# Kernel tuning notes

Hardware: AMD Instinct MI355X
Metric: run time of the kernel (lower is better)

## Reference

```python
import jax, jax.numpy as jnp
import numpy as np
from jax.ops import segment_sum, segment_max

N, E, H, C = 20000, 320000, 4, 128
G, NF, EF, GF = 1024, 9, 4, 50
EPS = 1e-5
NEG_SLOPE = 0.2


def setup_inputs() -> dict:
    key = jax.random.key(0)
    ks = jax.random.split(key, 16)
    inp = {
        'x': jax.random.normal(ks[0], (N, NF), jnp.float32),
        'edge_attr': jax.random.normal(ks[1], (E, EF), jnp.float32),
        'global_feat': jax.random.normal(ks[2], (G, GF), jnp.float32),
        'Wl1': jax.random.normal(ks[3], (NF, H * C), jnp.float32) * 0.1,
        'Wr1': jax.random.normal(ks[4], (NF, H * C), jnp.float32) * 0.1,
        'We1': jax.random.normal(ks[5], (EF, H * C), jnp.float32) * 0.1,
        'att1': jax.random.normal(ks[6], (H, C), jnp.float32) * 0.1,
        'b1': jax.random.normal(ks[7], (H * C,), jnp.float32) * 0.01,
        'gamma1': jnp.ones((H * C,), jnp.float32),
        'beta1': jnp.zeros((H * C,), jnp.float32),
        'mean1': jnp.zeros((H * C,), jnp.float32),
        'var1': jnp.ones((H * C,), jnp.float32),
        'Wl2': jax.random.normal(ks[8], (H * C, H * C), jnp.float32) * 0.05,
        'Wr2': jax.random.normal(ks[9], (H * C, H * C), jnp.float32) * 0.05,
        'We2': jax.random.normal(ks[10], (EF, H * C), jnp.float32) * 0.1,
        'att2': jax.random.normal(ks[11], (H, C), jnp.float32) * 0.1,
        'b2': jax.random.normal(ks[12], (H * C,), jnp.float32) * 0.01,
        'gamma2': jnp.ones((H * C,), jnp.float32),
        'beta2': jnp.zeros((H * C,), jnp.float32),
        'mean2': jnp.zeros((H * C,), jnp.float32),
        'var2': jnp.ones((H * C,), jnp.float32),
        'fc1_w': jax.random.normal(ks[13], (H * C + GF, C), jnp.float32) * 0.05,
        'fc1_b': jnp.zeros((C,), jnp.float32),
        'fc2_w': jax.random.normal(ks[14], (C, 1), jnp.float32) * 0.1,
        'fc2_b': jnp.zeros((1,), jnp.float32),
        'edge_index': jax.random.randint(ks[15], (2, E), 0, N, jnp.int32),
        'batch': jnp.sort(jax.random.randint(jax.random.fold_in(key, 99), (N,), 0, G, jnp.int32)),
    }
    return inp


def gatv2_layer(x, src, dst, ea, Wl, Wr, We, att, bias):
    # PyG GATv2Conv: add self-loops with fill_value='mean' edge_attr
    n = x.shape[0]
    loop = jnp.arange(n, dtype=src.dtype)
    deg = segment_sum(jnp.ones((src.shape[0],), x.dtype), dst, num_segments=n)
    ea_mean = segment_sum(ea, dst, num_segments=n) / jnp.clip(deg, 1.0)[:, None]
    s = jnp.concatenate([src, loop])
    d = jnp.concatenate([dst, loop])
    eat = jnp.concatenate([ea, ea_mean], axis=0)
    xl = (x @ Wl).reshape(n, H, C)  # source transform
    xr = (x @ Wr).reshape(n, H, C)  # target transform
    ee = (eat @ We).reshape(-1, H, C)
    e = jax.nn.leaky_relu(xl[s] + xr[d] + ee, NEG_SLOPE)  # [E+N, H, C]
    logits = jnp.einsum('ehc,hc->eh', e, att)  # [E+N, H]
    m = segment_max(logits, d, num_segments=n)  # stable segment softmax
    ex = jnp.exp(logits - m[d])
    alpha = ex / segment_sum(ex, d, num_segments=n)[d]
    out = segment_sum(alpha[..., None] * xl[s], d, num_segments=n)  # [N, H, C]
    return out.reshape(n, H * C) + bias


def batch_norm(x, g, b, mu, var):
    return (x - mu) * jax.lax.rsqrt(var + EPS) * g + b


def reference(x, edge_attr, global_feat, Wl1, Wr1, We1, att1, b1, gamma1, beta1, mean1, var1,
              Wl2, Wr2, We2, att2, b2, gamma2, beta2, mean2, var2,
              fc1_w, fc1_b, fc2_w, fc2_b, edge_index, batch):
    src, dst = edge_index[0], edge_index[1]
    h = jax.nn.relu(batch_norm(gatv2_layer(x, src, dst, edge_attr, Wl1, Wr1, We1, att1, b1),
                               gamma1, beta1, mean1, var1))
    h = jax.nn.relu(batch_norm(gatv2_layer(h, src, dst, edge_attr, Wl2, Wr2, We2, att2, b2),
                               gamma2, beta2, mean2, var2))
    cnt = segment_sum(jnp.ones((h.shape[0],), h.dtype), batch, num_segments=G)
    pooled = segment_sum(h, batch, num_segments=G) / jnp.clip(cnt, 1.0)[:, None]  # [G, H*C]
    z = jnp.concatenate([pooled, global_feat], axis=1)
    z = jax.nn.relu(z @ fc1_w + fc1_b)
    return (z @ fc2_w + fc2_b).squeeze()
```

## Files before the change

### kernel.cpp

```cpp
#include <hip/hip_runtime.h>
#include <hip/hip_bf16.h>

#define Nn 20000
#define Ee 320000
#define Hh 4
#define Cc 128
#define HC 512
#define Gg 1024
#define NFt 9
#define EFt 4
#define GFt 50
#define EPSf 1e-5f
#define SLOPE 0.2f

typedef __attribute__((ext_vector_type(8))) short bf16x8;
typedef __attribute__((ext_vector_type(4))) float f32x4;
typedef __attribute__((ext_vector_type(2))) float f32x2;
typedef __attribute__((ext_vector_type(4))) unsigned ui32x4;

typedef const __attribute__((address_space(1))) unsigned char* gp1_t;
typedef __attribute__((address_space(3))) unsigned char* lp3_t;
__device__ __forceinline__ void gload16(const void* g, void* l) {
    __builtin_amdgcn_global_load_lds((gp1_t)g, (lp3_t)l, 16, 0, 0);
}

__device__ __forceinline__ float bf2f(short s) {
    return __uint_as_float(((unsigned)(unsigned short)s) << 16);
}
__device__ __forceinline__ float rfl(float v) {
    return __uint_as_float(__builtin_amdgcn_readfirstlane(__float_as_uint(v)));
}

__device__ __forceinline__ f32x2 pkfma(f32x2 a, f32x2 b, f32x2 c) {
    f32x2 d;
    asm("v_pk_fma_f32 %0, %1, %2, %3" : "=v"(d) : "v"(a), "v"(b), "v"(c));
    return d;
}
__device__ __forceinline__ f32x2 pkadd(f32x2 a, f32x2 b) {
    f32x2 d;
    asm("v_pk_add_f32 %0, %1, %2" : "=v"(d) : "v"(a), "v"(b));
    return d;
}
__device__ __forceinline__ f32x2 pkmul(f32x2 a, f32x2 b) {
    f32x2 d;
    asm("v_pk_mul_f32 %0, %1, %2" : "=v"(d) : "v"(a), "v"(b));
    return d;
}

__global__ void k_setup2(const int* __restrict__ dst, int* __restrict__ deg,
                         const int* __restrict__ batch, int* __restrict__ gofs) {
    int b = blockIdx.x, t = threadIdx.x;
    if (b < 1250) {
        int e = b * 256 + t;
        if (e < Ee) atomicAdd(&deg[dst[e]], 1);
    } else {
        int i = (b - 1250) * 256 + t;
        if (i >= Nn) return;
        int bb = batch[i];
        if (i == 0) {
            for (int g = 0; g <= bb; ++g) gofs[g] = 0;
        } else {
            int bp = batch[i - 1];
            for (int g = bp + 1; g <= bb; ++g) gofs[g] = i;
        }
        if (i == Nn - 1) {
            for (int g = bb + 1; g <= Gg; ++g) gofs[g] = Nn;
        }
    }
}

__global__ __launch_bounds__(256) void k_cvtW(const float* __restrict__ Wl2,
                                              const float* __restrict__ Wr2,
                                              __hip_bfloat16* __restrict__ Wt) {
    __shared__ float tile[64][65];
    int tc = blockIdx.x * 64;
    int tk = blockIdx.y * 64;
    int t = threadIdx.x;
    int lc = t & 63, lr = t >> 6;
    const float* W = (tc < 512) ? Wl2 : Wr2;
    int cb = tc & 511;
#pragma unroll
    for (int i = 0; i < 16; ++i) {
        int r = lr * 16 + i;
        tile[r][lc] = W[(size_t)(tk + r) * 512 + cb + lc];
    }
    __syncthreads();
#pragma unroll
    for (int i = 0; i < 16; ++i) {
        int c = lr * 16 + i;
        Wt[(size_t)(tc + c) * 512 + tk + lc] = __float2bfloat16(tile[lc][c]);
    }
}

__global__ __launch_bounds__(256) void k_xlxr1(const float* __restrict__ x,
                                               const float* __restrict__ Wl1,
                                               const float* __restrict__ Wr1,
                                               __hip_bfloat16* __restrict__ xl,
                                               __hip_bfloat16* __restrict__ xr) {
    int t = threadIdx.x;
    int l = t & 63, w = t >> 6;
    int ch0 = l * 8;
    int wid = blockIdx.x * 4 + w;
    int n0 = wid * 2, n1 = n0 + 1;
    float xa[NFt], xb[NFt];
#pragma unroll
    for (int f = 0; f < NFt; ++f) {
        xa[f] = x[n0 * NFt + f];
        xb[f] = x[n1 * NFt + f];
    }
    float a0[8] = {}, r0[8] = {}, a1[8] = {}, r1[8] = {};
#pragma unroll
    for (int f = 0; f < NFt; ++f) {
        f32x4 wl0 = *(const f32x4*)&Wl1[f * HC + ch0];
        f32x4 wl1 = *(const f32x4*)&Wl1[f * HC + ch0 + 4];
        f32x4 wr0 = *(const f32x4*)&Wr1[f * HC + ch0];
        f32x4 wr1 = *(const f32x4*)&Wr1[f * HC + ch0 + 4];
#pragma unroll
        for (int k = 0; k < 4; ++k) {
            a0[k] = fmaf(xa[f], wl0[k], a0[k]);
            a0[k + 4] = fmaf(xa[f], wl1[k], a0[k + 4]);
            r0[k] = fmaf(xa[f], wr0[k], r0[k]);
            r0[k + 4] = fmaf(xa[f], wr1[k], r0[k + 4]);
            a1[k] = fmaf(xb[f], wl0[k], a1[k]);
            a1[k + 4] = fmaf(xb[f], wl1[k], a1[k + 4]);
            r1[k] = fmaf(xb[f], wr0[k], r1[k]);
            r1[k + 4] = fmaf(xb[f], wr1[k], r1[k + 4]);
        }
    }
    auto cvt8 = [](const float* v) {
        bf16x8 o;
#pragma unroll
        for (int k = 0; k < 8; ++k) {
            union { float f; unsigned u; } cv;
            cv.f = v[k];
            unsigned r = (cv.u + 0x7fff + ((cv.u >> 16) & 1)) >> 16;
            o[k] = (short)r;
        }
        return o;
    };
    *(bf16x8*)(xl + (size_t)n0 * HC + ch0) = cvt8(a0);
    *(bf16x8*)(xr + (size_t)n0 * HC + ch0) = cvt8(r0);
    *(bf16x8*)(xl + (size_t)n1 * HC + ch0) = cvt8(a1);
    *(bf16x8*)(xr + (size_t)n1 * HC + ch0) = cvt8(r1);
}

__global__ void k_scan(const int* __restrict__ deg, int* __restrict__ rowptr) {
    __shared__ int sums[1024];
    int t = threadIdx.x;
    const int n = Nn;
    int chunk = (n + 1023) / 1024;
    int start = t * chunk;
    int lim = min(start + chunk, n);
    int s = 0;
    for (int i = start; i < lim; ++i) s += deg[i];
    sums[t] = s;
    __syncthreads();
    for (int off = 1; off < 1024; off <<= 1) {
        int v = (t >= off) ? sums[t - off] : 0;
        __syncthreads();
        sums[t] += v;
        __syncthreads();
    }
    int run = (t == 0) ? 0 : sums[t - 1];
    for (int i = start; i < lim; ++i) { rowptr[i] = run; run += deg[i]; }
    if (t == 1023) rowptr[n] = sums[1023];
}

__global__ void k_scatter(const int* __restrict__ src, const int* __restrict__ dst,
                          const float* __restrict__ ea, const int* __restrict__ rowptr,
                          int* __restrict__ fill, int* __restrict__ csr_src,
                          float4* __restrict__ ea_s) {
    int e = blockIdx.x * 256 + threadIdx.x;
    if (e >= Ee) return;
    int d = dst[e];
    int pos = rowptr[d] + atomicAdd(&fill[d], 1);
    csr_src[pos] = src[e];
    ea_s[pos] = ((const float4*)ea)[e];
}

__global__ __launch_bounds__(256) void k_gemm_mfma(const short* __restrict__ Abf,
                                                   const short* __restrict__ Bt,
                                                   __hip_bfloat16* __restrict__ xl,
                                                   __hip_bfloat16* __restrict__ xr, int M) {
    __shared__ short As[128 * 32];
    __shared__ short Bs[128 * 32];
    int tid = threadIdx.x;
    int l = tid & 63;
    int wid = tid >> 6;
    int bm0 = blockIdx.x * 128;
    int bn0 = blockIdx.y * 128;
    int wr = (wid >> 1) * 64;
    int wc = (wid & 1) * 64;
    f32x4 acc[4][4] = {};

    int srow = l >> 2;
    int skoff = ((l & 3) ^ ((l >> 3) & 3)) * 8;
    int rk = (((l >> 4) ^ (l >> 1)) & 3) * 8;

    for (int k0 = 0; k0 < 512; k0 += 32) {
        {
            int c = wid;
            long row = min(bm0 + c * 16 + srow, M - 1);
            gload16(Abf + row * 512 + k0 + skoff, &As[c * 512]);
            int col = bn0 + c * 16 + srow;
            gload16(Bt + (size_t)col * 512 + k0 + skoff, &Bs[c * 512]);
            c = wid + 4;
            row = min(bm0 + c * 16 + srow, M - 1);
            gload16(Abf + row * 512 + k0 + skoff, &As[c * 512]);
            col = bn0 + c * 16 + srow;
            gload16(Bt + (size_t)col * 512 + k0 + skoff, &Bs[c * 512]);
        }
        asm volatile("s_waitcnt vmcnt(0)" ::: "memory");
        __syncthreads();
        bf16x8 af[4], bfr[4];
#pragma unroll
        for (int m = 0; m < 4; ++m)
            af[m] = *(const bf16x8*)&As[(wr + m * 16 + (l & 15)) * 32 + rk];
#pragma unroll
        for (int n = 0; n < 4; ++n)
            bfr[n] = *(const bf16x8*)&Bs[(wc + n * 16 + (l & 15)) * 32 + rk];
#pragma unroll
        for (int m = 0; m < 4; ++m)
#pragma unroll
            for (int n = 0; n < 4; ++n)
                acc[m][n] = __builtin_amdgcn_mfma_f32_16x16x32_bf16(af[m], bfr[n],
                                                                    acc[m][n], 0, 0, 0);
        __syncthreads();
    }
    __hip_bfloat16* dst = (bn0 < 512) ? xl : xr;
    int cb = bn0 & 511;
#pragma unroll
    for (int m = 0; m < 4; ++m) {
#pragma unroll
        for (int n = 0; n < 4; ++n) {
            int col = cb + wc + n * 16 + (l & 15);
#pragma unroll
            for (int r = 0; r < 4; ++r) {
                int row = bm0 + wr + m * 16 + (l >> 4) * 4 + r;
                if (row < M) dst[(size_t)row * 512 + col] = __float2bfloat16(acc[m][n][r]);
            }
        }
    }
}

__global__ __launch_bounds__(256) void k_fused_attn(
    const __hip_bfloat16* __restrict__ xl, const __hip_bfloat16* __restrict__ xr,
    const float* __restrict__ We, const float* __restrict__ att,
    const int* __restrict__ rowptr, const int* __restrict__ csr_src,
    const float4* __restrict__ ea_s, const float* __restrict__ bias,
    const float* __restrict__ gamma, const float* __restrict__ beta,
    const float* __restrict__ mean, const float* __restrict__ var,
    __hip_bfloat16* __restrict__ hout) {
    int n = blockIdx.x * 4 + (threadIdx.x >> 6);
    if (n >= Nn) return;
    int l = threadIdx.x & 63;
    int ch0 = l * 8;

    f32x2 wee2[4][4], ar2[4], rr2[4];
#pragma unroll
    for (int f = 0; f < 4; ++f) {
        f32x4 w0 = *(const f32x4*)&We[f * HC + ch0];
        f32x4 w1 = *(const f32x4*)&We[f * HC + ch0 + 4];
        wee2[f][0] = (f32x2){w0.x, w0.y};
        wee2[f][1] = (f32x2){w0.z, w0.w};
        wee2[f][2] = (f32x2){w1.x, w1.y};
        wee2[f][3] = (f32x2){w1.z, w1.w};
    }
    {
        f32x4 a0 = *(const f32x4*)&att[ch0];
        f32x4 a1 = *(const f32x4*)&att[ch0 + 4];
        ar2[0] = (f32x2){a0.x, a0.y};
        ar2[1] = (f32x2){a0.z, a0.w};
        ar2[2] = (f32x2){a1.x, a1.y};
        ar2[3] = (f32x2){a1.z, a1.w};
    }
    {
        ui32x4 ru = *(const ui32x4*)(xr + (size_t)n * HC + ch0);
#pragma unroll
        for (int j = 0; j < 4; ++j) {
            unsigned u = ru[j];
            rr2[j] = (f32x2){__uint_as_float(u << 16), __uint_as_float(u & 0xffff0000u)};
        }
    }

    int start = rowptr[n];
    int nedge = rowptr[n + 1] - start;
    int last = start + nedge - 1;

    float m = -1e30f, den = 0.f;
    f32x2 acc2[4] = {};
    float es0 = 0.f, es1 = 0.f, es2 = 0.f, es3 = 0.f;

    struct Chunk {
        int s[4];
        float e[4][4];
        bf16x8 x[4];
    };

    auto accum4 = [&](const Chunk& c, const float* ex) {
#pragma unroll
        for (int i = 0; i < 4; ++i) {
            f32x2 esp = (f32x2){ex[i], ex[i]};
            ui32x4 xu = *(const ui32x4*)&c.x[i];
#pragma unroll
            for (int j = 0; j < 4; ++j) {
                unsigned u = xu[j];
                f32x2 xv = (f32x2){__uint_as_float(u << 16),
                                   __uint_as_float(u & 0xffff0000u)};
                acc2[j] = pkfma(esp, xv, acc2[j]);
            }
        }
    };

    auto step = [&](Chunk& cur, Chunk& nxt, int base) {
#pragma unroll
        for (int i = 0; i < 4; ++i) {
            int idx = min(start + base + 4 + i, last);
            nxt.s[i] = __builtin_amdgcn_readfirstlane(csr_src[idx]);
            float4 v = ea_s[idx];
            nxt.e[i][0] = rfl(v.x); nxt.e[i][1] = rfl(v.y);
            nxt.e[i][2] = rfl(v.z); nxt.e[i][3] = rfl(v.w);
        }
#pragma unroll
        for (int i = 0; i < 4; ++i)
            nxt.x[i] = *(const bf16x8*)(xl + (size_t)nxt.s[i] * HC + ch0);

#pragma unroll
        for (int i = 0; i < 4; ++i) {
            if (base + i < nedge) {
                es0 += cur.e[i][0]; es1 += cur.e[i][1];
                es2 += cur.e[i][2]; es3 += cur.e[i][3];
            }
        }

        float p[4];
#pragma unroll
        for (int i = 0; i < 4; ++i) {
            ui32x4 xu = *(const ui32x4*)&cur.x[i];
            f32x2 es0p = (f32x2){cur.e[i][0], cur.e[i][0]};
            f32x2 es1p = (f32x2){cur.e[i][1], cur.e[i][1]};
            f32x2 es2p = (f32x2){cur.e[i][2], cur.e[i][2]};
            f32x2 es3p = (f32x2){cur.e[i][3], cur.e[i][3]};
            f32x2 plin = (f32x2){0.f, 0.f}, pabs = (f32x2){0.f, 0.f};
#pragma unroll
            for (int j = 0; j < 4; ++j) {
                unsigned u = xu[j];
                f32x2 xv = (f32x2){__uint_as_float(u << 16),
                                   __uint_as_float(u & 0xffff0000u)};
                f32x2 z = pkadd(xv, rr2[j]);
                z = pkfma(es0p, wee2[0][j], z);
                z = pkfma(es1p, wee2[1][j], z);
                z = pkfma(es2p, wee2[2][j], z);
                z = pkfma(es3p, wee2[3][j], z);
                f32x2 za = (f32x2){fabsf(z.x), fabsf(z.y)};
                plin = pkfma(ar2[j], z, plin);
                pabs = pkfma(ar2[j], za, pabs);
            }
            p[i] = 0.6f * (plin.x + plin.y) + 0.4f * (pabs.x + pabs.y);
        }
#pragma unroll
        for (int off = 8; off; off >>= 1) {
            p[0] += __shfl_xor(p[0], off);
            p[1] += __shfl_xor(p[1], off);
            p[2] += __shfl_xor(p[2], off);
            p[3] += __shfl_xor(p[3], off);
        }
#pragma unroll
        for (int i = 1; i < 4; ++i)
            if (base + i >= nedge) p[i] = -1e30f;

        float pmax = fmaxf(fmaxf(p[0], p[1]), fmaxf(p[2], p[3]));
        float ex[4];
        if (__all(pmax <= m + 8.f)) {
            ex[0] = __expf(p[0] - m); ex[1] = __expf(p[1] - m);
            ex[2] = __expf(p[2] - m); ex[3] = __expf(p[3] - m);
            den += ex[0] + ex[1] + ex[2] + ex[3];
            accum4(cur, ex);
        } else {
            float mn = fmaxf(m, pmax);
            float sc = __expf(m - mn);
            ex[0] = __expf(p[0] - mn); ex[1] = __expf(p[1] - mn);
            ex[2] = __expf(p[2] - mn); ex[3] = __expf(p[3] - mn);
            den = den * sc + ex[0] + ex[1] + ex[2] + ex[3];
            f32x2 scs = (f32x2){sc, sc};
#pragma unroll
            for (int j = 0; j < 4; ++j) acc2[j] = pkmul(acc2[j], scs);
            accum4(cur, ex);
            m = mn;
        }
    };

    if (nedge > 0) {
        Chunk A, B;
#pragma unroll
        for (int i = 0; i < 4; ++i) {
            int idx = min(start + i, last);
            A.s[i] = __builtin_amdgcn_readfirstlane(csr_src[idx]);
            float4 v = ea_s[idx];
            A.e[i][0] = rfl(v.x); A.e[i][1] = rfl(v.y);
            A.e[i][2] = rfl(v.z); A.e[i][3] = rfl(v.w);
        }
#pragma unroll
        for (int i = 0; i < 4; ++i)
            A.x[i] = *(const bf16x8*)(xl + (size_t)A.s[i] * HC + ch0);

        int base = 0;
        for (;;) {
            step(A, B, base);
            base += 4;
            if (base >= nedge) break;
            step(B, A, base);
            base += 4;
            if (base >= nedge) break;
        }
    }

    {
        float dv = (float)max(nedge, 1);
        float e0 = es0 / dv, e1 = es1 / dv, e2 = es2 / dv, e3 = es3 / dv;
        ui32x4 xu = *(const ui32x4*)(xl + (size_t)n * HC + ch0);
        f32x2 es0p = (f32x2){e0, e0}, es1p = (f32x2){e1, e1};
        f32x2 es2p = (f32x2){e2, e2}, es3p = (f32x2){e3, e3};
        f32x2 plin = (f32x2){0.f, 0.f}, pabs = (f32x2){0.f, 0.f};
        f32x2 xv2[4];
#pragma unroll
        for (int j = 0; j < 4; ++j) {
            unsigned u = xu[j];
            xv2[j] = (f32x2){__uint_as_float(u << 16), __uint_as_float(u & 0xffff0000u)};
            f32x2 z = pkadd(xv2[j], rr2[j]);
            z = pkfma(es0p, wee2[0][j], z);
            z = pkfma(es1p, wee2[1][j], z);
            z = pkfma(es2p, wee2[2][j], z);
            z = pkfma(es3p, wee2[3][j], z);
            f32x2 za = (f32x2){fabsf(z.x), fabsf(z.y)};
            plin = pkfma(ar2[j], z, plin);
            pabs = pkfma(ar2[j], za, pabs);
        }
        float pi = 0.6f * (plin.x + plin.y) + 0.4f * (pabs.x + pabs.y);
#pragma unroll
        for (int off = 8; off; off >>= 1) pi += __shfl_xor(pi, off);
        float mn = fmaxf(m, pi);
        float sc = __expf(m - mn);
        float ex = __expf(pi - mn);
        den = den * sc + ex;
        f32x2 scs = (f32x2){sc, sc};
        f32x2 exs = (f32x2){ex, ex};
#pragma unroll
        for (int j = 0; j < 4; ++j) acc2[j] = pkfma(exs, xv2[j], pkmul(acc2[j], scs));
    }

    float iden = 1.f / den;
    f32x4 bi0 = *(const f32x4*)&bias[ch0], bi1 = *(const f32x4*)&bias[ch0 + 4];
    f32x4 ga0 = *(const f32x4*)&gamma[ch0], ga1 = *(const f32x4*)&gamma[ch0 + 4];
    f32x4 be0 = *(const f32x4*)&beta[ch0], be1 = *(const f32x4*)&beta[ch0 + 4];
    f32x4 me0 = *(const f32x4*)&mean[ch0], me1 = *(const f32x4*)&mean[ch0 + 4];
    f32x4 va0 = *(const f32x4*)&var[ch0], va1 = *(const f32x4*)&var[ch0 + 4];
    float aflat[8] = {acc2[0].x, acc2[0].y, acc2[1].x, acc2[1].y,
                      acc2[2].x, acc2[2].y, acc2[3].x, acc2[3].y};
    bf16x8 ob;
#pragma unroll
    for (int k = 0; k < 8; ++k) {
        float bik = (k < 4) ? bi0[k] : bi1[k - 4];
        float gak = (k < 4) ? ga0[k] : ga1[k - 4];
        float bek = (k < 4) ? be0[k] : be1[k - 4];
        float mek = (k < 4) ? me0[k] : me1[k - 4];
        float vak = (k < 4) ? va0[k] : va1[k - 4];
        float v = aflat[k] * iden + bik;
        v = fmaxf((v - mek) * rsqrtf(vak + EPSf) * gak + bek, 0.f);
        union { float f; unsigned u; } cv;
        cv.f = v;
        unsigned r = (cv.u + 0x7fff + ((cv.u >> 16) & 1)) >> 16;
        ob[k] = (short)r;
    }
    *(bf16x8*)(hout + (size_t)n * HC + ch0) = ob;
}

__global__ __launch_bounds__(256) void k_pool_mlp(
    const __hip_bfloat16* __restrict__ h, const int* __restrict__ gofs,
    const float* __restrict__ gfeat, const float* __restrict__ fc1w,
    const float* __restrict__ fc1b, const float* __restrict__ fc2w,
    const float* __restrict__ fc2b, float* __restrict__ out) {
    __shared__ float z[HC + GFt];
    __shared__ float red[256];
    int g = blockIdx.x, t = threadIdx.x;
    int s = gofs[g], e = gofs[g + 1];
    float a0 = 0.f, a1 = 0.f;
    for (int r = s; r < e; ++r) {
        ushort2 v = ((const ushort2*)(h + (size_t)r * HC))[t];
        a0 += bf2f((short)v.x);
        a1 += bf2f((short)v.y);
    }
    float ic = (e > s) ? 1.f / (float)(e - s) : 0.f;
    z[2 * t] = a0 * ic;
    z[2 * t + 1] = a1 * ic;
    if (t < GFt) z[HC + t] = gfeat[g * GFt + t];
    __syncthreads();
    int c = t & 127, half = t >> 7;
    float acc = (half == 0) ? fc1b[c] : 0.f;
    int j0 = half * 281, j1 = j0 + 281;
    for (int j = j0; j < j1; ++j) acc += z[j] * fc1w[j * 128 + c];
    red[t] = acc;
    __syncthreads();
    if (t < 128) {
        float a = red[t] + red[t + 128];
        red[t] = fmaxf(a, 0.f) * fc2w[t];
    }
    __syncthreads();
    for (int off = 64; off; off >>= 1) {
        if (t < off) red[t] += red[t + off];
        __syncthreads();
    }
    if (t == 0) out[g] = red[0] + fc2b[0];
}

extern "C" void kernel_launch(void* const* d_in, const int* in_sizes, int n_in,
                              void* d_out, int out_size, void* d_ws, size_t ws_size,
                              hipStream_t stream) {
    const float* x = (const float*)d_in[0];
    const float* ea = (const float*)d_in[1];
    const float* gfeat = (const float*)d_in[2];
    const float* Wl1 = (const float*)d_in[3];
    const float* Wr1 = (const float*)d_in[4];
    const float* We1 = (const float*)d_in[5];
    const float* att1 = (const float*)d_in[6];
    const float* b1 = (const float*)d_in[7];
    const float* gamma1 = (const float*)d_in[8];
    const float* beta1 = (const float*)d_in[9];
    const float* mean1 = (const float*)d_in[10];
    const float* var1 = (const float*)d_in[11];
    const float* Wl2 = (const float*)d_in[12];
    const float* Wr2 = (const float*)d_in[13];
    const float* We2 = (const float*)d_in[14];
    const float* att2 = (const float*)d_in[15];
    const float* b2 = (const float*)d_in[16];
    const float* gamma2 = (const float*)d_in[17];
    const float* beta2 = (const float*)d_in[18];
    const float* mean2 = (const float*)d_in[19];
    const float* var2 = (const float*)d_in[20];
    const float* fc1w = (const float*)d_in[21];
    const float* fc1b = (const float*)d_in[22];
    const float* fc2w = (const float*)d_in[23];
    const float* fc2b = (const float*)d_in[24];
    const int* eidx = (const int*)d_in[25];
    const int* batch = (const int*)d_in[26];
    float* out = (float*)d_out;

    const int* srcp = eidx;
    const int* dstp = eidx + Ee;

    char* p = (char*)d_ws;
    auto alloc = [&](size_t bytes) -> char* {
        char* r = p;
        p += (bytes + 255) & ~(size_t)255;
        return r;
    };
    __hip_bfloat16* xl = (__hip_bfloat16*)alloc((size_t)Nn * HC * 2);
    __hip_bfloat16* xr = (__hip_bfloat16*)alloc((size_t)Nn * HC * 2);
    __hip_bfloat16* h_bf = (__hip_bfloat16*)alloc((size_t)Nn * HC * 2);
    int* deg = (int*)alloc((size_t)Nn * 4);
    int* fill = (int*)alloc((size_t)Nn * 4);
    int* rowptr = (int*)alloc((size_t)(Nn + 1) * 4);
    int* csr_src = (int*)alloc((size_t)Ee * 4);
    float4* ea_s = (float4*)alloc((size_t)Ee * 16);
    int* gofs = (int*)alloc((size_t)(Gg + 1) * 4);
    __hip_bfloat16* Wt = (__hip_bfloat16*)alloc((size_t)1024 * 512 * 2);

    hipMemsetAsync(deg, 0, (size_t)Nn * 4, stream);
    hipMemsetAsync(fill, 0, (size_t)Nn * 4, stream);

    k_setup2<<<1250 + 79, 256, 0, stream>>>(dstp, deg, batch, gofs);
    k_scan<<<1, 1024, 0, stream>>>(deg, rowptr);
    k_scatter<<<(Ee + 255) / 256, 256, 0, stream>>>(srcp, dstp, ea, rowptr, fill,
                                                    csr_src, ea_s);
    k_cvtW<<<dim3(16, 8), 256, 0, stream>>>(Wl2, Wr2, Wt);
    k_xlxr1<<<2500, 256, 0, stream>>>(x, Wl1, Wr1, xl, xr);

    k_fused_attn<<<(Nn + 3) / 4, 256, 0, stream>>>(xl, xr, We1, att1, rowptr, csr_src,
                                                   ea_s, b1, gamma1, beta1, mean1,
                                                   var1, h_bf);

    k_gemm_mfma<<<dim3((Nn + 127) / 128, 8), 256, 0, stream>>>(
        (const short*)h_bf, (const short*)Wt, xl, xr, Nn);
    k_fused_attn<<<(Nn + 3) / 4, 256, 0, stream>>>(xl, xr, We2, att2, rowptr, csr_src,
                                                   ea_s, b2, gamma2, beta2, mean2,
                                                   var2, h_bf);

    k_pool_mlp<<<Gg, 256, 0, stream>>>(h_bf, gofs, gfeat, fc1w, fc1b, fc2w, fc2b, out);
}
```

Measured before the change: 330.9 us.

## Persistent attention waves, rank-based CSR scatter, and merged setup kernels

Result: no change. 324.7 us (-1.9%).

```diff
diff --git a/kernel.cpp b/kernel.cpp
--- a/kernel.cpp
+++ b/kernel.cpp
@@ -12,6 +12,7 @@
 #define GFt 50
 #define EPSf 1e-5f
 #define SLOPE 0.2f
+#define NWAVES 4096
 
 typedef __attribute__((ext_vector_type(8))) short bf16x8;
 typedef __attribute__((ext_vector_type(4))) float f32x4;
@@ -47,13 +48,20 @@
     return d;
 }
 
-__global__ void k_setup2(const int* __restrict__ dst, int* __restrict__ deg,
-                         const int* __restrict__ batch, int* __restrict__ gofs) {
+__global__ __launch_bounds__(256) void k_setup(
+    const int* __restrict__ dst, int* __restrict__ deg, int* __restrict__ rank,
+    const int* __restrict__ batch, int* __restrict__ gofs,
+    const float* __restrict__ Wl2, const float* __restrict__ Wr2,
+    __hip_bfloat16* __restrict__ Wt,
+    const float* __restrict__ x, const float* __restrict__ Wl1,
+    const float* __restrict__ Wr1, __hip_bfloat16* __restrict__ xl,
+    __hip_bfloat16* __restrict__ xr) {
+    __shared__ float tile[64][65];
     int b = blockIdx.x, t = threadIdx.x;
     if (b < 1250) {
         int e = b * 256 + t;
-        if (e < Ee) atomicAdd(&deg[dst[e]], 1);
-    } else {
+        if (e < Ee) rank[e] = atomicAdd(&deg[dst[e]], 1);
+    } else if (b < 1329) {
         int i = (b - 1250) * 256 + t;
         if (i >= Nn) return;
         int bb = batch[i];
@@ -66,82 +74,70 @@
         if (i == Nn - 1) {
             for (int g = bb + 1; g <= Gg; ++g) gofs[g] = Nn;
         }
-    }
-}
-
-__global__ __launch_bounds__(256) void k_cvtW(const float* __restrict__ Wl2,
-                                              const float* __restrict__ Wr2,
-                                              __hip_bfloat16* __restrict__ Wt) {
-    __shared__ float tile[64][65];
-    int tc = blockIdx.x * 64;
-    int tk = blockIdx.y * 64;
-    int t = threadIdx.x;
-    int lc = t & 63, lr = t >> 6;
-    const float* W = (tc < 512) ? Wl2 : Wr2;
-    int cb = tc & 511;
-#pragma unroll
-    for (int i = 0; i < 16; ++i) {
-        int r = lr * 16 + i;
-        tile[r][lc] = W[(size_t)(tk + r) * 512 + cb + lc];
-    }
-    __syncthreads();
-#pragma unroll
-    for (int i = 0; i < 16; ++i) {
-        int c = lr * 16 + i;
-        Wt[(size_t)(tc + c) * 512 + tk + lc] = __float2bfloat16(tile[lc][c]);
-    }
-}
-
-__global__ __launch_bounds__(256) void k_xlxr1(const float* __restrict__ x,
-                                               const float* __restrict__ Wl1,
-                                               const float* __restrict__ Wr1,
-                                               __hip_bfloat16* __restrict__ xl,
-                                               __hip_bfloat16* __restrict__ xr) {
-    int t = threadIdx.x;
-    int l = t & 63, w = t >> 6;
-    int ch0 = l * 8;
-    int wid = blockIdx.x * 4 + w;
-    int n0 = wid * 2, n1 = n0 + 1;
-    float xa[NFt], xb[NFt];
-#pragma unroll
-    for (int f = 0; f < NFt; ++f) {
-        xa[f] = x[n0 * NFt + f];
-        xb[f] = x[n1 * NFt + f];
-    }
-    float a0[8] = {}, r0[8] = {}, a1[8] = {}, r1[8] = {};
-#pragma unroll
-    for (int f = 0; f < NFt; ++f) {
-        f32x4 wl0 = *(const f32x4*)&Wl1[f * HC + ch0];
-        f32x4 wl1 = *(const f32x4*)&Wl1[f * HC + ch0 + 4];
-        f32x4 wr0 = *(const f32x4*)&Wr1[f * HC + ch0];
-        f32x4 wr1 = *(const f32x4*)&Wr1[f * HC + ch0 + 4];
-#pragma unroll
-        for (int k = 0; k < 4; ++k) {
-            a0[k] = fmaf(xa[f], wl0[k], a0[k]);
-            a0[k + 4] = fmaf(xa[f], wl1[k], a0[k + 4]);
-            r0[k] = fmaf(xa[f], wr0[k], r0[k]);
-            r0[k + 4] = fmaf(xa[f], wr1[k], r0[k + 4]);
-            a1[k] = fmaf(xb[f], wl0[k], a1[k]);
-            a1[k + 4] = fmaf(xb[f], wl1[k], a1[k + 4]);
-            r1[k] = fmaf(xb[f], wr0[k], r1[k]);
-            r1[k + 4] = fmaf(xb[f], wr1[k], r1[k + 4]);
-        }
-    }
-    auto cvt8 = [](const float* v) {
-        bf16x8 o;
-#pragma unroll
-        for (int k = 0; k < 8; ++k) {
-            union { float f; unsigned u; } cv;
-            cv.f = v[k];
-            unsigned r = (cv.u + 0x7fff + ((cv.u >> 16) & 1)) >> 16;
-            o[k] = (short)r;
-        }
-        return o;
-    };
-    *(bf16x8*)(xl + (size_t)n0 * HC + ch0) = cvt8(a0);
-    *(bf16x8*)(xr + (size_t)n0 * HC + ch0) = cvt8(r0);
-    *(bf16x8*)(xl + (size_t)n1 * HC + ch0) = cvt8(a1);
-    *(bf16x8*)(xr + (size_t)n1 * HC + ch0) = cvt8(r1);
+    } else if (b < 1457) {
+        int tid = b - 1329;
+        int tc = (tid >> 3) * 64;
+        int tk = (tid & 7) * 64;
+        int lc = t & 63, lr = t >> 6;
+        const float* W = (tc < 512) ? Wl2 : Wr2;
+        int cb = tc & 511;
+#pragma unroll
+        for (int i = 0; i < 16; ++i) {
+            int r = lr * 16 + i;
+            tile[r][lc] = W[(size_t)(tk + r) * 512 + cb + lc];
+        }
+        __syncthreads();
+#pragma unroll
+        for (int i = 0; i < 16; ++i) {
+            int c = lr * 16 + i;
+            Wt[(size_t)(tc + c) * 512 + tk + lc] = __float2bfloat16(tile[lc][c]);
+        }
+    } else {
+        int l = t & 63, w = t >> 6;
+        int ch0 = l * 8;
+        int wid = (b - 1457) * 4 + w;
+        int n0 = wid * 2, n1 = n0 + 1;
+        float xa[NFt], xb[NFt];
+#pragma unroll
+        for (int f = 0; f < NFt; ++f) {
+            xa[f] = x[n0 * NFt + f];
+            xb[f] = x[n1 * NFt + f];
+        }
+        float a0[8] = {}, r0[8] = {}, a1[8] = {}, r1[8] = {};
+#pragma unroll
+        for (int f = 0; f < NFt; ++f) {
+            f32x4 wl0 = *(const f32x4*)&Wl1[f * HC + ch0];
+            f32x4 wl1 = *(const f32x4*)&Wl1[f * HC + ch0 + 4];
+            f32x4 wr0 = *(const f32x4*)&Wr1[f * HC + ch0];
+            f32x4 wr1 = *(const f32x4*)&Wr1[f * HC + ch0 + 4];
+#pragma unroll
+            for (int k = 0; k < 4; ++k) {
+                a0[k] = fmaf(xa[f], wl0[k], a0[k]);
+                a0[k + 4] = fmaf(xa[f], wl1[k], a0[k + 4]);
+                r0[k] = fmaf(xa[f], wr0[k], r0[k]);
+                r0[k + 4] = fmaf(xa[f], wr1[k], r0[k + 4]);
+                a1[k] = fmaf(xb[f], wl0[k], a1[k]);
+                a1[k + 4] = fmaf(xb[f], wl1[k], a1[k + 4]);
+                r1[k] = fmaf(xb[f], wr0[k], r1[k]);
+                r1[k + 4] = fmaf(xb[f], wr1[k], r1[k + 4]);
+            }
+        }
+        auto cvt8 = [](const float* v) {
+            bf16x8 o;
+#pragma unroll
+            for (int k = 0; k < 8; ++k) {
+                union { float f; unsigned u; } cv;
+                cv.f = v[k];
+                unsigned r = (cv.u + 0x7fff + ((cv.u >> 16) & 1)) >> 16;
+                o[k] = (short)r;
+            }
+            return o;
+        };
+        *(bf16x8*)(xl + (size_t)n0 * HC + ch0) = cvt8(a0);
+        *(bf16x8*)(xr + (size_t)n0 * HC + ch0) = cvt8(r0);
+        *(bf16x8*)(xl + (size_t)n1 * HC + ch0) = cvt8(a1);
+        *(bf16x8*)(xr + (size_t)n1 * HC + ch0) = cvt8(r1);
+    }
 }
 
 __global__ void k_scan(const int* __restrict__ deg, int* __restrict__ rowptr) {
@@ -168,12 +164,11 @@
 
 __global__ void k_scatter(const int* __restrict__ src, const int* __restrict__ dst,
                           const float* __restrict__ ea, const int* __restrict__ rowptr,
-                          int* __restrict__ fill, int* __restrict__ csr_src,
+                          const int* __restrict__ rank, int* __restrict__ csr_src,
                           float4* __restrict__ ea_s) {
     int e = blockIdx.x * 256 + threadIdx.x;
     if (e >= Ee) return;
-    int d = dst[e];
-    int pos = rowptr[d] + atomicAdd(&fill[d], 1);
+    int pos = rowptr[dst[e]] + rank[e];
     csr_src[pos] = src[e];
     ea_s[pos] = ((const float4*)ea)[e];
 }
@@ -251,12 +246,13 @@
     const float* __restrict__ gamma, const float* __restrict__ beta,
     const float* __restrict__ mean, const float* __restrict__ var,
     __hip_bfloat16* __restrict__ hout) {
-    int n = blockIdx.x * 4 + (threadIdx.x >> 6);
-    if (n >= Nn) return;
     int l = threadIdx.x & 63;
+    int wid = __builtin_amdgcn_readfirstlane(blockIdx.x * 4 + (threadIdx.x >> 6));
     int ch0 = l * 8;
-
-    f32x2 wee2[4][4], ar2[4], rr2[4];
+    int nA = (int)(((long)wid * Nn) / NWAVES);
+    int nB = (int)(((long)(wid + 1) * Nn) / NWAVES);
+
+    f32x2 wee2[4][4], ar2[4];
 #pragma unroll
     for (int f = 0; f < 4; ++f) {
         f32x4 w0 = *(const f32x4*)&We[f * HC + ch0];
@@ -274,80 +270,182 @@
         ar2[2] = (f32x2){a1.x, a1.y};
         ar2[3] = (f32x2){a1.z, a1.w};
     }
+    float S[8], O[8];
     {
-        ui32x4 ru = *(const ui32x4*)(xr + (size_t)n * HC + ch0);
-#pragma unroll
-        for (int j = 0; j < 4; ++j) {
-            unsigned u = ru[j];
-            rr2[j] = (f32x2){__uint_as_float(u << 16), __uint_as_float(u & 0xffff0000u)};
-        }
-    }
-
-    int start = rowptr[n];
-    int nedge = rowptr[n + 1] - start;
-    int last = start + nedge - 1;
-
-    float m = -1e30f, den = 0.f;
-    f32x2 acc2[4] = {};
-    float es0 = 0.f, es1 = 0.f, es2 = 0.f, es3 = 0.f;
-
-    struct Chunk {
-        int s[4];
-        float e[4][4];
-        bf16x8 x[4];
-    };
-
-    auto accum4 = [&](const Chunk& c, const float* ex) {
-#pragma unroll
-        for (int i = 0; i < 4; ++i) {
-            f32x2 esp = (f32x2){ex[i], ex[i]};
-            ui32x4 xu = *(const ui32x4*)&c.x[i];
+        f32x4 bi0 = *(const f32x4*)&bias[ch0], bi1 = *(const f32x4*)&bias[ch0 + 4];
+        f32x4 ga0 = *(const f32x4*)&gamma[ch0], ga1 = *(const f32x4*)&gamma[ch0 + 4];
+        f32x4 be0 = *(const f32x4*)&beta[ch0], be1 = *(const f32x4*)&beta[ch0 + 4];
+        f32x4 me0 = *(const f32x4*)&mean[ch0], me1 = *(const f32x4*)&mean[ch0 + 4];
+        f32x4 va0 = *(const f32x4*)&var[ch0], va1 = *(const f32x4*)&var[ch0 + 4];
+#pragma unroll
+        for (int k = 0; k < 8; ++k) {
+            float bik = (k < 4) ? bi0[k] : bi1[k - 4];
+            float gak = (k < 4) ? ga0[k] : ga1[k - 4];
+            float bek = (k < 4) ? be0[k] : be1[k - 4];
+            float mek = (k < 4) ? me0[k] : me1[k - 4];
+            float vak = (k < 4) ? va0[k] : va1[k - 4];
+            S[k] = gak * rsqrtf(vak + EPSf);
+            O[k] = (bik - mek) * S[k] + bek;
+        }
+    }
+
+    for (int n = nA; n < nB; ++n) {
+        f32x2 rr2[4];
+        {
+            ui32x4 ru = *(const ui32x4*)(xr + (size_t)n * HC + ch0);
+#pragma unroll
+            for (int j = 0; j < 4; ++j) {
+                unsigned u = ru[j];
+                rr2[j] = (f32x2){__uint_as_float(u << 16),
+                                 __uint_as_float(u & 0xffff0000u)};
+            }
+        }
+        int start = __builtin_amdgcn_readfirstlane(rowptr[n]);
+        int nedge = __builtin_amdgcn_readfirstlane(rowptr[n + 1]) - start;
+        int last = start + nedge - 1;
+
+        float m = -1e30f, den = 0.f;
+        f32x2 acc2[4] = {};
+        float es0 = 0.f, es1 = 0.f, es2 = 0.f, es3 = 0.f;
+
+        struct Chunk {
+            int s[4];
+            float e[4][4];
+            bf16x8 x[4];
+        };
+
+        auto accum4 = [&](const Chunk& c, const float* ex) {
+#pragma unroll
+            for (int i = 0; i < 4; ++i) {
+                f32x2 esp = (f32x2){ex[i], ex[i]};
+                ui32x4 xu = *(const ui32x4*)&c.x[i];
+#pragma unroll
+                for (int j = 0; j < 4; ++j) {
+                    unsigned u = xu[j];
+                    f32x2 xv = (f32x2){__uint_as_float(u << 16),
+                                       __uint_as_float(u & 0xffff0000u)};
+                    acc2[j] = pkfma(esp, xv, acc2[j]);
+                }
+            }
+        };
+
+        auto step = [&](Chunk& cur, Chunk& nxt, int base) {
+#pragma unroll
+            for (int i = 0; i < 4; ++i) {
+                int idx = __builtin_amdgcn_readfirstlane(min(start + base + 4 + i, last));
+                nxt.s[i] = __builtin_amdgcn_readfirstlane(csr_src[idx]);
+                float4 v = ea_s[idx];
+                nxt.e[i][0] = rfl(v.x); nxt.e[i][1] = rfl(v.y);
+                nxt.e[i][2] = rfl(v.z); nxt.e[i][3] = rfl(v.w);
+            }
+#pragma unroll
+            for (int i = 0; i < 4; ++i)
+                nxt.x[i] = *(const bf16x8*)(xl + (size_t)nxt.s[i] * HC + ch0);
+
+#pragma unroll
+            for (int i = 0; i < 4; ++i) {
+                if (base + i < nedge) {
+                    es0 += cur.e[i][0]; es1 += cur.e[i][1];
+                    es2 += cur.e[i][2]; es3 += cur.e[i][3];
+                }
+            }
+
+            float p[4];
+#pragma unroll
+            for (int i = 0; i < 4; ++i) {
+                ui32x4 xu = *(const ui32x4*)&cur.x[i];
+                f32x2 es0p = (f32x2){cur.e[i][0], cur.e[i][0]};
+                f32x2 es1p = (f32x2){cur.e[i][1], cur.e[i][1]};
+                f32x2 es2p = (f32x2){cur.e[i][2], cur.e[i][2]};
+                f32x2 es3p = (f32x2){cur.e[i][3], cur.e[i][3]};
+                f32x2 plin = (f32x2){0.f, 0.f}, pabs = (f32x2){0.f, 0.f};
+#pragma unroll
+                for (int j = 0; j < 4; ++j) {
+                    unsigned u = xu[j];
+                    f32x2 xv = (f32x2){__uint_as_float(u << 16),
+                                       __uint_as_float(u & 0xffff0000u)};
+                    f32x2 z = pkadd(xv, rr2[j]);
+                    z = pkfma(es0p, wee2[0][j], z);
+                    z = pkfma(es1p, wee2[1][j], z);
+                    z = pkfma(es2p, wee2[2][j], z);
+                    z = pkfma(es3p, wee2[3][j], z);
+                    f32x2 za = (f32x2){fabsf(z.x), fabsf(z.y)};
+                    plin = pkfma(ar2[j], z, plin);
+                    pabs = pkfma(ar2[j], za, pabs);
+                }
+                p[i] = 0.6f * (plin.x + plin.y) + 0.4f * (pabs.x + pabs.y);
+            }
+#pragma unroll
+            for (int off = 8; off; off >>= 1) {
+                p[0] += __shfl_xor(p[0], off);
+                p[1] += __shfl_xor(p[1], off);
+                p[2] += __shfl_xor(p[2], off);
+                p[3] += __shfl_xor(p[3], off);
+            }
+#pragma unroll
+            for (int i = 1; i < 4; ++i)
+                if (base + i >= nedge) p[i] = -1e30f;
+
+            float pmax = fmaxf(fmaxf(p[0], p[1]), fmaxf(p[2], p[3]));
+            float ex[4];
+            if (__all(pmax <= m + 8.f)) {
+                ex[0] = __expf(p[0] - m); ex[1] = __expf(p[1] - m);
+                ex[2] = __expf(p[2] - m); ex[3] = __expf(p[3] - m);
+                den += ex[0] + ex[1] + ex[2] + ex[3];
+                accum4(cur, ex);
+            } else {
+                float mn = fmaxf(m, pmax);
+                float sc = __expf(m - mn);
+                ex[0] = __expf(p[0] - mn); ex[1] = __expf(p[1] - mn);
+                ex[2] = __expf(p[2] - mn); ex[3] = __expf(p[3] - mn);
+                den = den * sc + ex[0] + ex[1] + ex[2] + ex[3];
+                f32x2 scs = (f32x2){sc, sc};
+#pragma unroll
+                for (int j = 0; j < 4; ++j) acc2[j] = pkmul(acc2[j], scs);
+                accum4(cur, ex);
+                m = mn;
+            }
+        };
+
+        if (nedge > 0) {
+            Chunk A, B;
+#pragma unroll
+            for (int i = 0; i < 4; ++i) {
+                int idx = __builtin_amdgcn_readfirstlane(min(start + i, last));
+                A.s[i] = __builtin_amdgcn_readfirstlane(csr_src[idx]);
+                float4 v = ea_s[idx];
+                A.e[i][0] = rfl(v.x); A.e[i][1] = rfl(v.y);
+                A.e[i][2] = rfl(v.z); A.e[i][3] = rfl(v.w);
+            }
+#pragma unroll
+            for (int i = 0; i < 4; ++i)
+                A.x[i] = *(const bf16x8*)(xl + (size_t)A.s[i] * HC + ch0);
+
+            int base = 0;
+            for (;;) {
+                step(A, B, base);
+                base += 4;
+                if (base >= nedge) break;
+                step(B, A, base);
+                base += 4;
+                if (base >= nedge) break;
+            }
+        }
+
+        {
+            float dv = (float)max(nedge, 1);
+            float e0 = es0 / dv, e1 = es1 / dv, e2 = es2 / dv, e3 = es3 / dv;
+            ui32x4 xu = *(const ui32x4*)(xl + (size_t)n * HC + ch0);
+            f32x2 es0p = (f32x2){e0, e0}, es1p = (f32x2){e1, e1};
+            f32x2 es2p = (f32x2){e2, e2}, es3p = (f32x2){e3, e3};
+            f32x2 plin = (f32x2){0.f, 0.f}, pabs = (f32x2){0.f, 0.f};
+            f32x2 xv2[4];
 #pragma unroll
             for (int j = 0; j < 4; ++j) {
                 unsigned u = xu[j];
-                f32x2 xv = (f32x2){__uint_as_float(u << 16),
-                                   __uint_as_float(u & 0xffff0000u)};
-                acc2[j] = pkfma(esp, xv, acc2[j]);
-            }
-        }
-    };
-
-    auto step = [&](Chunk& cur, Chunk& nxt, int base) {
-#pragma unroll
-        for (int i = 0; i < 4; ++i) {
-            int idx = min(start + base + 4 + i, last);
-            nxt.s[i] = __builtin_amdgcn_readfirstlane(csr_src[idx]);
-            float4 v = ea_s[idx];
-            nxt.e[i][0] = rfl(v.x); nxt.e[i][1] = rfl(v.y);
-            nxt.e[i][2] = rfl(v.z); nxt.e[i][3] = rfl(v.w);
-        }
-#pragma unroll
-        for (int i = 0; i < 4; ++i)
-            nxt.x[i] = *(const bf16x8*)(xl + (size_t)nxt.s[i] * HC + ch0);
-
-#pragma unroll
-        for (int i = 0; i < 4; ++i) {
-            if (base + i < nedge) {
-                es0 += cur.e[i][0]; es1 += cur.e[i][1];
-                es2 += cur.e[i][2]; es3 += cur.e[i][3];
-            }
-        }
-
-        float p[4];
-#pragma unroll
-        for (int i = 0; i < 4; ++i) {
-            ui32x4 xu = *(const ui32x4*)&cur.x[i];
-            f32x2 es0p = (f32x2){cur.e[i][0], cur.e[i][0]};
-            f32x2 es1p = (f32x2){cur.e[i][1], cur.e[i][1]};
-            f32x2 es2p = (f32x2){cur.e[i][2], cur.e[i][2]};
-            f32x2 es3p = (f32x2){cur.e[i][3], cur.e[i][3]};
-            f32x2 plin = (f32x2){0.f, 0.f}, pabs = (f32x2){0.f, 0.f};
-#pragma unroll
-            for (int j = 0; j < 4; ++j) {
-                unsigned u = xu[j];
-                f32x2 xv = (f32x2){__uint_as_float(u << 16),
-                                   __uint_as_float(u & 0xffff0000u)};
-                f32x2 z = pkadd(xv, rr2[j]);
+                xv2[j] = (f32x2){__uint_as_float(u << 16),
+                                 __uint_as_float(u & 0xffff0000u)};
+                f32x2 z = pkadd(xv2[j], rr2[j]);
                 z = pkfma(es0p, wee2[0][j], z);
                 z = pkfma(es1p, wee2[1][j], z);
                 z = pkfma(es2p, wee2[2][j], z);
@@ -356,123 +454,34 @@
                 plin = pkfma(ar2[j], z, plin);
                 pabs = pkfma(ar2[j], za, pabs);
             }
-            p[i] = 0.6f * (plin.x + plin.y) + 0.4f * (pabs.x + pabs.y);
-        }
-#pragma unroll
-        for (int off = 8; off; off >>= 1) {
-            p[0] += __shfl_xor(p[0], off);
-            p[1] += __shfl_xor(p[1], off);
-            p[2] += __shfl_xor(p[2], off);
-            p[3] += __shfl_xor(p[3], off);
-        }
-#pragma unroll
-        for (int i = 1; i < 4; ++i)
-            if (base + i >= nedge) p[i] = -1e30f;
-
-        float pmax = fmaxf(fmaxf(p[0], p[1]), fmaxf(p[2], p[3]));
-        float ex[4];
-        if (__all(pmax <= m + 8.f)) {
-            ex[0] = __expf(p[0] - m); ex[1] = __expf(p[1] - m);
-            ex[2] = __expf(p[2] - m); ex[3] = __expf(p[3] - m);
-            den += ex[0] + ex[1] + ex[2] + ex[3];
-            accum4(cur, ex);
-        } else {
-            float mn = fmaxf(m, pmax);
+            float pi = 0.6f * (plin.x + plin.y) + 0.4f * (pabs.x + pabs.y);
+#pragma unroll
+            for (int off = 8; off; off >>= 1) pi += __shfl_xor(pi, off);
+            float mn = fmaxf(m, pi);
             float sc = __expf(m - mn);
-            ex[0] = __expf(p[0] - mn); ex[1] = __expf(p[1] - mn);
-            ex[2] = __expf(p[2] - mn); ex[3] = __expf(p[3] - mn);
-            den = den * sc + ex[0] + ex[1] + ex[2] + ex[3];
+            float ex = __expf(pi - mn);
+            den = den * sc + ex;
             f32x2 scs = (f32x2){sc, sc};
-#pragma unroll
-            for (int j = 0; j < 4; ++j) acc2[j] = pkmul(acc2[j], scs);
-            accum4(cur, ex);
-            m = mn;
-        }
-    };
-
-    if (nedge > 0) {
-        Chunk A, B;
-#pragma unroll
-        for (int i = 0; i < 4; ++i) {
-            int idx = min(start + i, last);
-            A.s[i] = __builtin_amdgcn_readfirstlane(csr_src[idx]);
-            float4 v = ea_s[idx];
-            A.e[i][0] = rfl(v.x); A.e[i][1] = rfl(v.y);
-            A.e[i][2] = rfl(v.z); A.e[i][3] = rfl(v.w);
-        }
-#pragma unroll
-        for (int i = 0; i < 4; ++i)
-            A.x[i] = *(const bf16x8*)(xl + (size_t)A.s[i] * HC + ch0);
-
-        int base = 0;
-        for (;;) {
-            step(A, B, base);
-            base += 4;
-            if (base >= nedge) break;
-            step(B, A, base);
-            base += 4;
-            if (base >= nedge) break;
-        }
-    }
-
-    {
-        float dv = (float)max(nedge, 1);
-        float e0 = es0 / dv, e1 = es1 / dv, e2 = es2 / dv, e3 = es3 / dv;
-        ui32x4 xu = *(const ui32x4*)(xl + (size_t)n * HC + ch0);
-        f32x2 es0p = (f32x2){e0, e0}, es1p = (f32x2){e1, e1};
-        f32x2 es2p = (f32x2){e2, e2}, es3p = (f32x2){e3, e3};
-        f32x2 plin = (f32x2){0.f, 0.f}, pabs = (f32x2){0.f, 0.f};
-        f32x2 xv2[4];
-#pragma unroll
-        for (int j = 0; j < 4; ++j) {
-            unsigned u = xu[j];
-            xv2[j] = (f32x2){__uint_as_float(u << 16), __uint_as_float(u & 0xffff0000u)};
-            f32x2 z = pkadd(xv2[j], rr2[j]);
-            z = pkfma(es0p, wee2[0][j], z);
-            z = pkfma(es1p, wee2[1][j], z);
-            z = pkfma(es2p, wee2[2][j], z);
-            z = pkfma(es3p, wee2[3][j], z);
-            f32x2 za = (f32x2){fabsf(z.x), fabsf(z.y)};
-            plin = pkfma(ar2[j], z, plin);
-            pabs = pkfma(ar2[j], za, pabs);
-        }
-        float pi = 0.6f * (plin.x + plin.y) + 0.4f * (pabs.x + pabs.y);
-#pragma unroll
-        for (int off = 8; off; off >>= 1) pi += __shfl_xor(pi, off);
-        float mn = fmaxf(m, pi);
-        float sc = __expf(m - mn);
-        float ex = __expf(pi - mn);
-        den = den * sc + ex;
-        f32x2 scs = (f32x2){sc, sc};
-        f32x2 exs = (f32x2){ex, ex};
-#pragma unroll
-        for (int j = 0; j < 4; ++j) acc2[j] = pkfma(exs, xv2[j], pkmul(acc2[j], scs));
-    }
-
-    float iden = 1.f / den;
-    f32x4 bi0 = *(const f32x4*)&bias[ch0], bi1 = *(const f32x4*)&bias[ch0 + 4];
-    f32x4 ga0 = *(const f32x4*)&gamma[ch0], ga1 = *(const f32x4*)&gamma[ch0 + 4];
-    f32x4 be0 = *(const f32x4*)&beta[ch0], be1 = *(const f32x4*)&beta[ch0 + 4];
-    f32x4 me0 = *(const f32x4*)&mean[ch0], me1 = *(const f32x4*)&mean[ch0 + 4];
-    f32x4 va0 = *(const f32x4*)&var[ch0], va1 = *(const f32x4*)&var[ch0 + 4];
-    float aflat[8] = {acc2[0].x, acc2[0].y, acc2[1].x, acc2[1].y,
-                      acc2[2].x, acc2[2].y, acc2[3].x, acc2[3].y};
-    bf16x8 ob;
-#pragma unroll
-    for (int k = 0; k < 8; ++k) {
-        float bik = (k < 4) ? bi0[k] : bi1[k - 4];
-        float gak = (k < 4) ? ga0[k] : ga1[k - 4];
-        float bek = (k < 4) ? be0[k] : be1[k - 4];
-        float mek = (k < 4) ? me0[k] : me1[k - 4];
-        float vak = (k < 4) ? va0[k] : va1[k - 4];
-        float v = aflat[k] * iden + bik;
-        v = fmaxf((v - mek) * rsqrtf(vak + EPSf) * gak + bek, 0.f);
-        union { float f; unsigned u; } cv;
-        cv.f = v;
-        unsigned r = (cv.u + 0x7fff + ((cv.u >> 16) & 1)) >> 16;
-        ob[k] = (short)r;
-    }
-    *(bf16x8*)(hout + (size_t)n * HC + ch0) = ob;
+            f32x2 exs = (f32x2){ex, ex};
+#pragma unroll
+            for (int j = 0; j < 4; ++j)
+                acc2[j] = pkfma(exs, xv2[j], pkmul(acc2[j], scs));
+        }
+
+        float iden = 1.f / den;
+        float aflat[8] = {acc2[0].x, acc2[0].y, acc2[1].x, acc2[1].y,
+                          acc2[2].x, acc2[2].y, acc2[3].x, acc2[3].y};
+        bf16x8 ob;
+#pragma unroll
+        for (int k = 0; k < 8; ++k) {
+            float v = fmaxf(fmaf(aflat[k] * iden, S[k], O[k]), 0.f);
+            union { float f; unsigned u; } cv;
+            cv.f = v;
+            unsigned r = (cv.u + 0x7fff + ((cv.u >> 16) & 1)) >> 16;
+            ob[k] = (short)r;
+        }
+        *(bf16x8*)(hout + (size_t)n * HC + ch0) = ob;
+    }
 }
 
 __global__ __launch_bounds__(256) void k_pool_mlp(
@@ -558,7 +567,7 @@
     __hip_bfloat16* xr = (__hip_bfloat16*)alloc((size_t)Nn * HC * 2);
     __hip_bfloat16* h_bf = (__hip_bfloat16*)alloc((size_t)Nn * HC * 2);
     int* deg = (int*)alloc((size_t)Nn * 4);
-    int* fill = (int*)alloc((size_t)Nn * 4);
+    int* rank = (int*)alloc((size_t)Ee * 4);
     int* rowptr = (int*)alloc((size_t)(Nn + 1) * 4);
     int* csr_src = (int*)alloc((size_t)Ee * 4);
     float4* ea_s = (float4*)alloc((size_t)Ee * 16);
@@ -566,24 +575,22 @@
     __hip_bfloat16* Wt = (__hip_bfloat16*)alloc((size_t)1024 * 512 * 2);
 
     hipMemsetAsync(deg, 0, (size_t)Nn * 4, stream);
-    hipMemsetAsync(fill, 0, (size_t)Nn * 4, stream);
-
-    k_setup2<<<1250 + 79, 256, 0, stream>>>(dstp, deg, batch, gofs);
+
+    k_setup<<<1457 + 2500, 256, 0, stream>>>(dstp, deg, rank, batch, gofs, Wl2, Wr2,
+                                             Wt, x, Wl1, Wr1, xl, xr);
     k_scan<<<1, 1024, 0, stream>>>(deg, rowptr);
-    k_scatter<<<(Ee + 255) / 256, 256, 0, stream>>>(srcp, dstp, ea, rowptr, fill,
+    k_scatter<<<(Ee + 255) / 256, 256, 0, stream>>>(srcp, dstp, ea, rowptr, rank,
                                                     csr_src, ea_s);
-    k_cvtW<<<dim3(16, 8), 256, 0, stream>>>(Wl2, Wr2, Wt);
-    k_xlxr1<<<2500, 256, 0, stream>>>(x, Wl1, Wr1, xl, xr);
-
-    k_fused_attn<<<(Nn + 3) / 4, 256, 0, stream>>>(xl, xr, We1, att1, rowptr, csr_src,
-                                                   ea_s, b1, gamma1, beta1, mean1,
-                                                   var1, h_bf);
+
+    k_fused_attn<<<NWAVES / 4, 256, 0, stream>>>(xl, xr, We1, att1, rowptr, csr_src,
+                                                 ea_s, b1, gamma1, beta1, mean1, var1,
+                                                 h_bf);
 
     k_gemm_mfma<<<dim3((Nn + 127) / 128, 8), 256, 0, stream>>>(
         (const short*)h_bf, (const short*)Wt, xl, xr, Nn);
-    k_fused_attn<<<(Nn + 3) / 4, 256, 0, stream>>>(xl, xr, We2, att2, rowptr, csr_src,
-                                                   ea_s, b2, gamma2, beta2, mean2,
-                                                   var2, h_bf);
+    k_fused_attn<<<NWAVES / 4, 256, 0, stream>>>(xl, xr, We2, att2, rowptr, csr_src,
+                                                 ea_s, b2, gamma2, beta2, mean2, var2,
+                                                 h_bf);
 
     k_pool_mlp<<<Gg, 256, 0, stream>>>(h_bf, gofs, gfeat, fc1w, fc1b, fc2w, fc2b, out);
 }
```
